# Kernel optimization log

Hardware: AMD Instinct MI355X
Metric: run time of the kernel (lower is better)

Reference implementation:

```python
import jax, jax.numpy as jnp
import numpy as np

COMMITMENT_COST = 0.25


def setup_inputs() -> dict:
    key = jax.random.key(0)
    k1, k2 = jax.random.split(key)
    x = jax.random.normal(k1, (16, 2048, 256), dtype=jnp.float32)
    # stacked per-layer codebooks: [num_quantizers, num_embeddings, embedding_dim]
    embeddings = jax.random.normal(k2, (8, 1024, 256), dtype=jnp.float32)
    return {"x": x, "embeddings": embeddings}


def reference(x, embeddings):
    """Residual VQ forward (eval mode: no EMA update, no quantizer dropout).

    x: [B, T, D]; embeddings: [L, K, D].
    Returns (quantized_out [B,T,D], loss scalar, codes [B,T,L]).
    """
    B, T, D = x.shape
    L, K, _ = embeddings.shape
    flat = x.reshape(-1, D)                      # [N, D], N = B*T
    quantized_out = jnp.zeros_like(flat)
    residual = flat
    loss = jnp.float32(0.0)
    codes = []
    for l in range(L):                           # small fixed layer loop
        emb = embeddings[l]                      # [K, D]
        # pairwise squared distances [N, K]
        dist = (jnp.sum(residual * residual, axis=1, keepdims=True)
                + jnp.sum(emb * emb, axis=1)
                - 2.0 * residual @ emb.T)
        idx = jnp.argmin(dist, axis=1)           # [N]
        q = emb[idx]                             # gather [N, D]
        # commitment loss uses pre-STE quantized (detached) vs layer input
        loss = loss + COMMITMENT_COST * jnp.mean(
            (jax.lax.stop_gradient(q) - residual) ** 2)
        # straight-through estimator
        q_st = residual + jax.lax.stop_gradient(q - residual)
        quantized_out = quantized_out + q_st
        residual = residual - q_st
        codes.append(idx)
    codes = jnp.stack(codes, axis=1).reshape(B, T, L)
    return quantized_out.reshape(B, T, D), loss, codes
```

## Files before the change

### kernel.cpp

```cpp
#include <hip/hip_runtime.h>


#define NL 8
#define NK 1024
#define ND 256
#define NROWTOT 32768
#define ROWS 32
#define RSTR 260
#define KT 256
#define DT 16
#define ESTR 20

__global__ __launch_bounds__(256)
void enorm_zero_kernel(const float* __restrict__ emb, float* __restrict__ enorm,
                       float* __restrict__ loss_slot) {
    int row = blockIdx.x * 32 + (threadIdx.x >> 3);
    int l8  = threadIdx.x & 7;
    const float4* e4 = (const float4*)(emb + (size_t)row * ND);
    float s = 0.f;
#pragma unroll
    for (int q = 0; q < 8; ++q) {
        float4 v = e4[q * 8 + l8];
        s = fmaf(v.x, v.x, s); s = fmaf(v.y, v.y, s);
        s = fmaf(v.z, v.z, s); s = fmaf(v.w, v.w, s);
    }
    s += __shfl_xor(s, 1);
    s += __shfl_xor(s, 2);
    s += __shfl_xor(s, 4);
    if (l8 == 0) enorm[row] = s;
    if (blockIdx.x == 0 && threadIdx.x == 0) *loss_slot = 0.f;
}

__global__ __launch_bounds__(256, 2)
void rvq_kernel(const float* __restrict__ x, const float* __restrict__ emb,
                const float* __restrict__ enorm, float* __restrict__ out) {
    __shared__ float R[ROWS][RSTR];
    __shared__ float Et[2][KT][ESTR];
    __shared__ float En[NK];
    __shared__ int   amin[ROWS];
    __shared__ float lred[4];

    const int tid   = threadIdx.x;
    const int tx    = tid & 63;
    const int ty    = tid >> 6;
    const int row_e = tid >> 3;
    const int dq    = tid & 7;
    const int sk    = tid >> 2;
    const int sq    = tid & 3;
    const int brow  = blockIdx.x * ROWS;

    float* loss_slot = out + (size_t)NROWTOT * ND;
    float* codes     = loss_slot + 1;

    const float4* x4 = (const float4*)(x + (size_t)(brow + row_e) * ND);
#pragma unroll
    for (int q = 0; q < 8; ++q) {
        int qq = q * 8 + dq;
        *(float4*)&R[row_e][qq * 4] = x4[qq];
    }

    const float4* emb4 = (const float4*)emb;
    float4 stage[4];
#pragma unroll
    for (int p = 0; p < 4; ++p)
        stage[p] = emb4[(size_t)(p * 64 + sk) * 64 + sq];
#pragma unroll
    for (int p = 0; p < 4; ++p)
        *(float4*)&Et[0][p * 64 + sk][sq * 4] = stage[p];
#pragma unroll
    for (int p = 0; p < 4; ++p)
        stage[p] = emb4[(size_t)(p * 64 + sk) * 64 + 4 + sq];

    float loss_acc = 0.f;

    for (int l = 0; l < NL; ++l) {
        const float* enl = enorm + l * NK;
#pragma unroll
        for (int p = 0; p < 4; ++p) En[tid + p * 256] = enl[tid + p * 256];

        float minv[8];
        int   mini[8];
#pragma unroll
        for (int i = 0; i < 8; ++i) { minv[i] = 3.4e38f; mini[i] = 0; }

        float acc[8][4];

        for (int cc = 0; cc < 64; ++cc) {
            const int g   = l * 64 + cc;
            const int kc  = cc >> 4, dc = cc & 15;
            const int buf = g & 1;

            __syncthreads();
#pragma unroll
            for (int p = 0; p < 4; ++p)
                *(float4*)&Et[buf ^ 1][p * 64 + sk][sq * 4] = stage[p];
            {
                int gp = g + 2; if (gp > 511) gp = 511;
                const int lp = gp >> 6, kcp = (gp >> 4) & 3, dcp = gp & 15;
                const size_t base = (size_t)lp * 65536
                                  + (size_t)(kcp * KT + sk) * 64
                                  + (size_t)dcp * 4 + sq;
#pragma unroll
                for (int p = 0; p < 4; ++p)
                    stage[p] = emb4[base + (size_t)(p * 64) * 64];
            }
            if (dc == 0) {
#pragma unroll
                for (int i = 0; i < 8; ++i)
#pragma unroll
                    for (int j = 0; j < 4; ++j) acc[i][j] = 0.f;
            }
#pragma unroll
            for (int dd = 0; dd < DT; dd += 4) {
                float4 rv[8];
#pragma unroll
                for (int i = 0; i < 8; ++i)
                    rv[i] = *(const float4*)&R[ty * 8 + i][dc * DT + dd];
#pragma unroll
                for (int j = 0; j < 4; ++j) {
                    float4 ev = *(const float4*)&Et[buf][tx + 64 * j][dd];
#pragma unroll
                    for (int i = 0; i < 8; ++i) {
                        acc[i][j] = fmaf(rv[i].x, ev.x, acc[i][j]);
                        acc[i][j] = fmaf(rv[i].y, ev.y, acc[i][j]);
                        acc[i][j] = fmaf(rv[i].z, ev.z, acc[i][j]);
                        acc[i][j] = fmaf(rv[i].w, ev.w, acc[i][j]);
                    }
                }
            }
            if (dc == 15) {
#pragma unroll
                for (int j = 0; j < 4; ++j) {
                    int   kg = kc * KT + j * 64 + tx;
                    float en = En[kg];
#pragma unroll
                    for (int i = 0; i < 8; ++i) {
                        float dv = fmaf(-2.f, acc[i][j], en);
                        if (dv < minv[i]) { minv[i] = dv; mini[i] = kg; }
                    }
                }
            }
        }
#pragma unroll
        for (int off = 32; off >= 1; off >>= 1) {
#pragma unroll
            for (int i = 0; i < 8; ++i) {
                float ov = __shfl_xor(minv[i], off);
                int   oi = __shfl_xor(mini[i], off);
                if (ov < minv[i] || (ov == minv[i] && oi < mini[i])) {
                    minv[i] = ov; mini[i] = oi;
                }
            }
        }
        if (tx == 0) {
#pragma unroll
            for (int i = 0; i < 8; ++i) amin[ty * 8 + i] = mini[i];
        }
        __syncthreads();
        {
            const float* el = emb + (size_t)l * NK * ND;
            int idx = amin[row_e];
            const float4* q4 = (const float4*)(el + (size_t)idx * ND);
#pragma unroll
            for (int q = 0; q < 8; ++q) {
                int qq = q * 8 + dq;
                float4 qv = q4[qq];
                float4 rv = *(const float4*)&R[row_e][qq * 4];
                float4 df, qs, rn;
                df.x = qv.x - rv.x; df.y = qv.y - rv.y;
                df.z = qv.z - rv.z; df.w = qv.w - rv.w;
                loss_acc = fmaf(df.x, df.x, loss_acc);
                loss_acc = fmaf(df.y, df.y, loss_acc);
                loss_acc = fmaf(df.z, df.z, loss_acc);
                loss_acc = fmaf(df.w, df.w, loss_acc);
                qs.x = rv.x + df.x; qs.y = rv.y + df.y;
                qs.z = rv.z + df.z; qs.w = rv.w + df.w;
                rn.x = rv.x - qs.x; rn.y = rv.y - qs.y;
                rn.z = rv.z - qs.z; rn.w = rv.w - qs.w;
                *(float4*)&R[row_e][qq * 4] = rn;
            }
            if (dq == 0) codes[(size_t)(brow + row_e) * NL + l] = (float)idx;
        }
    }
#pragma unroll
    for (int q = 0; q < 8; ++q) {
        int qq = q * 8 + dq;
        float4 xv = x4[qq];
        float4 rv = *(const float4*)&R[row_e][qq * 4];
        float4 ov;
        ov.x = xv.x - rv.x; ov.y = xv.y - rv.y;
        ov.z = xv.z - rv.z; ov.w = xv.w - rv.w;
        ((float4*)(out + (size_t)(brow + row_e) * ND))[qq] = ov;
    }
#pragma unroll
    for (int off = 32; off >= 1; off >>= 1) loss_acc += __shfl_xor(loss_acc, off);
    if ((tid & 63) == 0) lred[tid >> 6] = loss_acc;
    __syncthreads();
    if (tid == 0) {
        float t = lred[0] + lred[1] + lred[2] + lred[3];
        atomicAdd(loss_slot, t * (0.25f / ((float)NROWTOT * (float)ND)));
    }
}

extern "C" void kernel_launch(void* const* d_in, const int* in_sizes, int n_in,
                              void* d_out, int out_size, void* d_ws, size_t ws_size,
                              hipStream_t stream) {
    const float* x   = (const float*)d_in[0];
    const float* emb = (const float*)d_in[1];
    float* out   = (float*)d_out;
    float* enorm = (float*)d_ws;
    float* loss_slot = out + (size_t)NROWTOT * ND;

    enorm_zero_kernel<<<256, 256, 0, stream>>>(emb, enorm, loss_slot);
    rvq_kernel<<<NROWTOT / ROWS, 256, 0, stream>>>(x, emb, enorm, out);
}
```

Before: 2.815 ms.

## Tile distance GEMM over all codes with four-wide depth slices

Restructures the per-layer distance computation so each thread keeps accumulators for all 1024 codes (8 rows x 16 codes) and loops over the embedding dimension in slices of 4. Each slice stages a float4 from every code into shared memory, replacing the 256-code by 16-dim tiles. The intent is to cut the chunk bookkeeping and to read each residual value once per slice for 16 codes instead of 4. The cost is 128 accumulator registers per thread at two blocks per SM, which risks spills or lower occupancy. Global loads also become strided by row (one float4 per 1 KB row), which may hurt coalescing.

New measurement: 3.269 ms. 16.1% more time.

```diff
diff --git a/kernel.cpp b/kernel.cpp
--- a/kernel.cpp
+++ b/kernel.cpp
@@ -7,9 +7,6 @@
 #define NROWTOT 32768
 #define ROWS 32
 #define RSTR 260
-#define KT 256
-#define DT 16
-#define ESTR 20
 
 __global__ __launch_bounds__(256)
 void enorm_zero_kernel(const float* __restrict__ emb, float* __restrict__ enorm,
@@ -34,19 +31,17 @@
 __global__ __launch_bounds__(256, 2)
 void rvq_kernel(const float* __restrict__ x, const float* __restrict__ emb,
                 const float* __restrict__ enorm, float* __restrict__ out) {
-    __shared__ float R[ROWS][RSTR];
-    __shared__ float Et[2][KT][ESTR];
-    __shared__ float En[NK];
-    __shared__ int   amin[ROWS];
-    __shared__ float lred[4];
+    __shared__ float  R[ROWS][RSTR];
+    __shared__ float4 Es[2][NK];
+    __shared__ float  En[NK];
+    __shared__ int    amin[ROWS];
+    __shared__ float  lred[4];
 
     const int tid   = threadIdx.x;
     const int tx    = tid & 63;
     const int ty    = tid >> 6;
     const int row_e = tid >> 3;
     const int dq    = tid & 7;
-    const int sk    = tid >> 2;
-    const int sq    = tid & 3;
     const int brow  = blockIdx.x * ROWS;
 
     float* loss_slot = out + (size_t)NROWTOT * ND;
@@ -63,13 +58,13 @@
     float4 stage[4];
 #pragma unroll
     for (int p = 0; p < 4; ++p)
-        stage[p] = emb4[(size_t)(p * 64 + sk) * 64 + sq];
+        stage[p] = emb4[(size_t)(tid + 256 * p) * 64];
 #pragma unroll
     for (int p = 0; p < 4; ++p)
-        *(float4*)&Et[0][p * 64 + sk][sq * 4] = stage[p];
+        Es[0][tid + 256 * p] = stage[p];
 #pragma unroll
     for (int p = 0; p < 4; ++p)
-        stage[p] = emb4[(size_t)(p * 64 + sk) * 64 + 4 + sq];
+        stage[p] = emb4[(size_t)(tid + 256 * p) * 64 + 1];
 
     float loss_acc = 0.f;
 
@@ -78,67 +73,56 @@
 #pragma unroll
         for (int p = 0; p < 4; ++p) En[tid + p * 256] = enl[tid + p * 256];
 
+        float acc[8][16];
+#pragma unroll
+        for (int i = 0; i < 8; ++i)
+#pragma unroll
+            for (int j = 0; j < 16; ++j) acc[i][j] = 0.f;
+
+        for (int dc = 0; dc < 64; ++dc) {
+            const int g   = l * 64 + dc;
+            const int buf = g & 1;
+
+            __syncthreads();
+#pragma unroll
+            for (int p = 0; p < 4; ++p)
+                Es[buf ^ 1][tid + 256 * p] = stage[p];
+            {
+                int gp = g + 2; if (gp > 511) gp = 511;
+                const int lp = gp >> 6, dcp = gp & 63;
+                const size_t base = (size_t)lp * 65536 + (size_t)tid * 64 + dcp;
+#pragma unroll
+                for (int p = 0; p < 4; ++p)
+                    stage[p] = emb4[base + (size_t)(p * 256) * 64];
+            }
+            float4 rv[8];
+#pragma unroll
+            for (int i = 0; i < 8; ++i)
+                rv[i] = *(const float4*)&R[ty * 8 + i][dc * 4];
+#pragma unroll
+            for (int j = 0; j < 16; ++j) {
+                float4 ev = Es[buf][j * 64 + tx];
+#pragma unroll
+                for (int i = 0; i < 8; ++i) {
+                    acc[i][j] = fmaf(rv[i].x, ev.x, acc[i][j]);
+                    acc[i][j] = fmaf(rv[i].y, ev.y, acc[i][j]);
+                    acc[i][j] = fmaf(rv[i].z, ev.z, acc[i][j]);
+                    acc[i][j] = fmaf(rv[i].w, ev.w, acc[i][j]);
+                }
+            }
+        }
         float minv[8];
         int   mini[8];
 #pragma unroll
         for (int i = 0; i < 8; ++i) { minv[i] = 3.4e38f; mini[i] = 0; }
-
-        float acc[8][4];
-
-        for (int cc = 0; cc < 64; ++cc) {
-            const int g   = l * 64 + cc;
-            const int kc  = cc >> 4, dc = cc & 15;
-            const int buf = g & 1;
-
-            __syncthreads();
-#pragma unroll
-            for (int p = 0; p < 4; ++p)
-                *(float4*)&Et[buf ^ 1][p * 64 + sk][sq * 4] = stage[p];
-            {
-                int gp = g + 2; if (gp > 511) gp = 511;
-                const int lp = gp >> 6, kcp = (gp >> 4) & 3, dcp = gp & 15;
-                const size_t base = (size_t)lp * 65536
-                                  + (size_t)(kcp * KT + sk) * 64
-                                  + (size_t)dcp * 4 + sq;
-#pragma unroll
-                for (int p = 0; p < 4; ++p)
-                    stage[p] = emb4[base + (size_t)(p * 64) * 64];
-            }
-            if (dc == 0) {
-#pragma unroll
-                for (int i = 0; i < 8; ++i)
-#pragma unroll
-                    for (int j = 0; j < 4; ++j) acc[i][j] = 0.f;
-            }
-#pragma unroll
-            for (int dd = 0; dd < DT; dd += 4) {
-                float4 rv[8];
-#pragma unroll
-                for (int i = 0; i < 8; ++i)
-                    rv[i] = *(const float4*)&R[ty * 8 + i][dc * DT + dd];
-#pragma unroll
-                for (int j = 0; j < 4; ++j) {
-                    float4 ev = *(const float4*)&Et[buf][tx + 64 * j][dd];
-#pragma unroll
-                    for (int i = 0; i < 8; ++i) {
-                        acc[i][j] = fmaf(rv[i].x, ev.x, acc[i][j]);
-                        acc[i][j] = fmaf(rv[i].y, ev.y, acc[i][j]);
-                        acc[i][j] = fmaf(rv[i].z, ev.z, acc[i][j]);
-                        acc[i][j] = fmaf(rv[i].w, ev.w, acc[i][j]);
-                    }
-                }
-            }
-            if (dc == 15) {
-#pragma unroll
-                for (int j = 0; j < 4; ++j) {
-                    int   kg = kc * KT + j * 64 + tx;
-                    float en = En[kg];
-#pragma unroll
-                    for (int i = 0; i < 8; ++i) {
-                        float dv = fmaf(-2.f, acc[i][j], en);
-                        if (dv < minv[i]) { minv[i] = dv; mini[i] = kg; }
-                    }
-                }
+#pragma unroll
+        for (int j = 0; j < 16; ++j) {
+            int   kg = j * 64 + tx;
+            float en = En[kg];
+#pragma unroll
+            for (int i = 0; i < 8; ++i) {
+                float dv = fmaf(-2.f, acc[i][j], en);
+                if (dv < minv[i]) { minv[i] = dv; mini[i] = kg; }
             }
         }
 #pragma unroll
```
